# Performance work log

Hardware: AMD Instinct MI355X
Metric: run time of the kernel (lower is better)

Reference implementation:

```python
import jax, jax.numpy as jnp
import numpy as np

D_MODEL = 1024
NUM_HEADS = 16
HEAD_DIM = D_MODEL // NUM_HEADS  # 64
SEQ = 2048
BATCH = 4
LN_EPS = 1e-5


def setup_inputs() -> dict:
    key = jax.random.key(0)
    k_in, k_qkv, k_o, k_g = jax.random.split(key, 4)
    inputs = jax.random.normal(k_in, (BATCH, SEQ, D_MODEL), dtype=jnp.float32)
    mask = jnp.zeros((BATCH, 1, SEQ, SEQ), dtype=jnp.float32)  # additive mask
    # Realistic rotary embeddings (RoPE), duplicated-halves layout
    inv_freq = 1.0 / (10000.0 ** (jnp.arange(0, HEAD_DIM, 2, dtype=jnp.float32) / HEAD_DIM))
    pos = jnp.arange(SEQ, dtype=jnp.float32)
    freqs = pos[:, None] * inv_freq[None, :]            # [S, Dh/2]
    emb = jnp.concatenate([freqs, freqs], axis=-1)       # [S, Dh]
    cos = jnp.cos(emb)
    sin = jnp.sin(emb)
    # Parameters
    sd = 1.0 / np.sqrt(D_MODEL)
    w_qkv = jax.random.normal(k_qkv, (D_MODEL, 3 * D_MODEL), dtype=jnp.float32) * sd
    w_o = jax.random.normal(k_o, (D_MODEL, D_MODEL), dtype=jnp.float32) * sd
    ln_gamma = jnp.ones((D_MODEL,), dtype=jnp.float32)
    return {"inputs": inputs, "mask": mask, "cos": cos, "sin": sin,
            "ln_gamma": ln_gamma, "w_qkv": w_qkv, "w_o": w_o}


def _rotate_half(x):
    x1, x2 = jnp.split(x, 2, axis=-1)
    return jnp.concatenate([-x2, x1], axis=-1)


def reference(inputs, mask, cos, sin, ln_gamma, w_qkv, w_o):
    B, S, D = inputs.shape
    # Pre-attention LayerNorm (layer_id != 0), center=False -> no beta
    mu = jnp.mean(inputs, axis=-1, keepdims=True)
    var = jnp.mean(jnp.square(inputs - mu), axis=-1, keepdims=True)
    x = (inputs - mu) / jnp.sqrt(var + LN_EPS) * ln_gamma
    # Fused QKV projection, split into heads: [B, H, S, Dh]
    qkv = (x @ w_qkv).reshape(B, S, 3, NUM_HEADS, HEAD_DIM)
    qkv = jnp.transpose(qkv, (2, 0, 3, 1, 4))
    q, k, v = qkv[0], qkv[1], qkv[2]
    # RoPE
    c = cos.reshape(1, 1, S, HEAD_DIM)
    s = sin.reshape(1, 1, S, HEAD_DIM)
    q = q * c + _rotate_half(q) * s
    k = k * c + _rotate_half(k) * s
    # Scaled dot-product attention with additive mask
    scale = 1.0 / jnp.sqrt(jnp.asarray(HEAD_DIM, dtype=q.dtype))
    logits = jnp.einsum("bhqd,bhkd->bhqk", q, k) * scale + mask
    attn = jax.nn.softmax(logits, axis=-1)
    out = jnp.einsum("bhqk,bhkd->bhqd", attn, v)
    out = jnp.transpose(out, (0, 2, 1, 3)).reshape(B, S, D)
    return out @ w_o
```

## Files before the change

kernel.cpp:

```cpp
#include <hip/hip_runtime.h>
#include <stdint.h>

#define DEV __device__ __forceinline__

typedef __bf16 bf16x8 __attribute__((ext_vector_type(8)));
typedef float f32x4 __attribute__((ext_vector_type(4)));
typedef float f32x16 __attribute__((ext_vector_type(16)));

DEV unsigned short f2bf(float f) {
  union { float f; uint32_t u; } c; c.f = f;
  uint32_t u = c.u;
  u += 0x7FFFu + ((u >> 16) & 1u);
  return (unsigned short)(u >> 16);
}
DEV float bf2f(unsigned short h) {
  union { uint32_t u; float f; } c; c.u = ((uint32_t)h) << 16;
  return c.f;
}
DEV float u2f(uint32_t u) {
  union { uint32_t u; float f; } c; c.u = u;
  return c.f;
}
DEV bf16x8 ld8(const unsigned short* p) {
  uint4 u = *reinterpret_cast<const uint4*>(p);
  return __builtin_bit_cast(bf16x8, u);
}
DEV uint32_t cvtpk(float lo, float hi) {
  uint32_t r;
  asm("v_cvt_pk_bf16_f32 %0, %1, %2" : "=v"(r) : "v"(lo), "v"(hi));
  return r;
}
DEV void permswap(uint32_t& a, uint32_t& b) {
  asm("v_permlane32_swap_b32 %0, %1" : "+v"(a), "+v"(b));
}
DEV float exp2b(float x) { return __builtin_amdgcn_exp2f(x); }
DEV void gload16(const void* g, void* l) {
  __builtin_amdgcn_global_load_lds((const __attribute__((address_space(1))) void*)g,
                                   (__attribute__((address_space(3))) void*)l, 16, 0, 0);
}

template<int K, int N>
__global__ __launch_bounds__(256)
void transpose_cast_kernel(const float* __restrict__ in, unsigned short* __restrict__ out) {
  __shared__ float tile[64][65];
  const int bk = blockIdx.x % (K / 64);
  const int bn = blockIdx.x / (K / 64);
  const int k0 = bk * 64, n0 = bn * 64;
  const int t = threadIdx.x;
#pragma unroll
  for (int i = 0; i < 16; ++i) {
    int idx = t + i * 256;
    int kl = idx >> 6, nl = idx & 63;
    tile[kl][nl] = in[(size_t)(k0 + kl) * N + n0 + nl];
  }
  __syncthreads();
#pragma unroll
  for (int i = 0; i < 16; ++i) {
    int idx = t + i * 256;
    int nl = idx >> 6, kl = idx & 63;
    out[(size_t)(n0 + nl) * K + k0 + kl] = f2bf(tile[kl][nl]);
  }
}

__global__ __launch_bounds__(256)
void ln_kernel(const float* __restrict__ x, const float* __restrict__ gamma,
               unsigned short* __restrict__ y) {
  const int row = blockIdx.x;
  const int t = threadIdx.x;
  const float4 v = reinterpret_cast<const float4*>(x + (size_t)row * 1024)[t];
  float s  = v.x + v.y + v.z + v.w;
  float s2 = v.x * v.x + v.y * v.y + v.z * v.z + v.w * v.w;
#pragma unroll
  for (int off = 1; off < 64; off <<= 1) {
    s  += __shfl_xor(s, off);
    s2 += __shfl_xor(s2, off);
  }
  __shared__ float red[8];
  const int w = t >> 6, lane = t & 63;
  if (lane == 0) { red[w] = s; red[4 + w] = s2; }
  __syncthreads();
  s  = red[0] + red[1] + red[2] + red[3];
  s2 = red[4] + red[5] + red[6] + red[7];
  const float mu = s * (1.0f / 1024.0f);
  const float var = s2 * (1.0f / 1024.0f) - mu * mu;
  const float rstd = rsqrtf(var + 1e-5f);
  const float4 g = reinterpret_cast<const float4*>(gamma)[t];
  ushort4 o;
  o.x = f2bf((v.x - mu) * rstd * g.x);
  o.y = f2bf((v.y - mu) * rstd * g.y);
  o.z = f2bf((v.z - mu) * rstd * g.z);
  o.w = f2bf((v.w - mu) * rstd * g.w);
  reinterpret_cast<ushort4*>(y + (size_t)row * 1024)[t] = o;
}

template<int N_DIM, bool OUT_F32>
__global__ __launch_bounds__(256)
void gemm_bt_kernel(const unsigned short* __restrict__ A,
                    const unsigned short* __restrict__ Bt,
                    void* __restrict__ Cout) {
  constexpr int K = 1024;
  __shared__ unsigned short a_lds[128 * 32];
  __shared__ unsigned short b_lds[128 * 32];
  const int t = threadIdx.x;
  const int w = t >> 6, l = t & 63;
  const int lrow = l & 15, lch = l >> 4;
  const int nbn = N_DIM / 128;
  const int m0 = (blockIdx.x / nbn) * 128;
  const int n0 = (blockIdx.x % nbn) * 128;
  const int wm = (w >> 1) * 64, wn = (w & 1) * 64;

  const int srow = t >> 2;
  const int schk = t & 3;
  const int scol = ((schk ^ (srow & 3)) << 3);
  const unsigned short* aS0 = A  + (size_t)(m0 + srow) * K + scol;
  const unsigned short* aS1 = A  + (size_t)(m0 + 64 + srow) * K + scol;
  const unsigned short* bS0 = Bt + (size_t)(n0 + srow) * K + scol;
  const unsigned short* bS1 = Bt + (size_t)(n0 + 64 + srow) * K + scol;
  unsigned short* aD0 = a_lds + (w * 16) * 32;
  unsigned short* aD1 = a_lds + (64 + w * 16) * 32;
  unsigned short* bD0 = b_lds + (w * 16) * 32;
  unsigned short* bD1 = b_lds + (64 + w * 16) * 32;

  f32x4 acc[4][4] = {};

  for (int k0 = 0; k0 < K; k0 += 32) {
    gload16(aS0 + k0, aD0);
    gload16(aS1 + k0, aD1);
    gload16(bS0 + k0, bD0);
    gload16(bS1 + k0, bD1);
    __syncthreads();
    bf16x8 af[4], bfr[4];
#pragma unroll
    for (int m = 0; m < 4; ++m) {
      int row = wm + m * 16 + lrow;
      af[m] = ld8(a_lds + row * 32 + ((lch ^ (lrow & 3)) << 3));
    }
#pragma unroll
    for (int n = 0; n < 4; ++n) {
      int row = wn + n * 16 + lrow;
      bfr[n] = ld8(b_lds + row * 32 + ((lch ^ (lrow & 3)) << 3));
    }
#pragma unroll
    for (int m = 0; m < 4; ++m)
#pragma unroll
      for (int n = 0; n < 4; ++n)
        acc[m][n] = __builtin_amdgcn_mfma_f32_16x16x32_bf16(af[m], bfr[n], acc[m][n], 0, 0, 0);
    __syncthreads();
  }

#pragma unroll
  for (int m = 0; m < 4; ++m) {
    const int grow0 = m0 + wm + m * 16 + lch * 4;
#pragma unroll
    for (int n = 0; n < 4; ++n) {
      const int gcol = n0 + wn + n * 16 + lrow;
#pragma unroll
      for (int r = 0; r < 4; ++r) {
        if constexpr (OUT_F32)
          ((float*)Cout)[(size_t)(grow0 + r) * N_DIM + gcol] = acc[m][n][r];
        else
          ((unsigned short*)Cout)[(size_t)(grow0 + r) * N_DIM + gcol] = f2bf(acc[m][n][r]);
      }
    }
  }
}

__global__ __launch_bounds__(256)
void rope_split_kernel(const unsigned short* __restrict__ qkv,
                       const float* __restrict__ cosb,
                       const float* __restrict__ sinb,
                       unsigned short* __restrict__ Qo,
                       unsigned short* __restrict__ Kf,
                       unsigned short* __restrict__ Vf) {
  const int bid = blockIdx.x;
  const int sb = bid & 31, h = (bid >> 5) & 15, b = bid >> 9;
  const int s0 = sb * 64;
  const int t = threadIdx.x;
  __shared__ unsigned short qt[64][72], kt[64][72], vt[64][72];

  const int sl = t >> 2, c0 = (t & 3) * 16;
  {
    const size_t base = (size_t)(b * 2048 + s0 + sl) * 3072 + h * 64 + c0;
    uint4 q1 = *(const uint4*)(qkv + base);
    uint4 q2 = *(const uint4*)(qkv + base + 8);
    uint4 k1 = *(const uint4*)(qkv + base + 1024);
    uint4 k2 = *(const uint4*)(qkv + base + 1032);
    uint4 v1 = *(const uint4*)(qkv + base + 2048);
    uint4 v2 = *(const uint4*)(qkv + base + 2056);
    *(uint4*)&qt[sl][c0] = q1; *(uint4*)&qt[sl][c0 + 8] = q2;
    *(uint4*)&kt[sl][c0] = k1; *(uint4*)&kt[sl][c0 + 8] = k2;
    *(uint4*)&vt[sl][c0] = v1; *(uint4*)&vt[sl][c0 + 8] = v2;
  }
  __syncthreads();
  const size_t fbase = (size_t)(b * 16 + h) * 131072;
  {
    const int sg = s0 + sl;
    alignas(16) unsigned short qo16[16], ko16[16];
#pragma unroll
    for (int j = 0; j < 16; ++j) {
      const int d = c0 + j;
      const float cv = cosb[sg * 64 + d], sv = sinb[sg * 64 + d];
      const float qv = bf2f(qt[sl][d]), qp = bf2f(qt[sl][d ^ 32]);
      const float kv = bf2f(kt[sl][d]), kp = bf2f(kt[sl][d ^ 32]);
      const float rq = qv * cv + ((d < 32) ? -qp : qp) * sv;
      const float rk = kv * cv + ((d < 32) ? -kp : kp) * sv;
      qo16[j] = f2bf(rq * 0.180336880f);
      ko16[j] = f2bf(rk);
    }
    const size_t ob = ((size_t)(b * 16 + h) * 2048 + sg) * 64 + c0;
    *(uint4*)(Qo + ob) = *(uint4*)qo16; *(uint4*)(Qo + ob + 8) = *(uint4*)(qo16 + 8);
    unsigned short* kd = Kf + fbase + ((size_t)((sb * 2 + (sl >> 5)) * 4 + (t & 3))) * 512;
    *(uint4*)(kd + (sl & 31) * 8)        = *(uint4*)ko16;
    *(uint4*)(kd + (32 + (sl & 31)) * 8) = *(uint4*)(ko16 + 8);
  }
  {
    const int dh = t >> 2, sc0 = (t & 3) * 16;
    alignas(16) unsigned short vo16[16];
#pragma unroll
    for (int j = 0; j < 16; ++j) vo16[j] = vt[sc0 + j][dh];
    unsigned short* vd = Vf + fbase + ((size_t)((sb * 2 + (dh >> 5)) * 4 + (t & 3))) * 512;
    *(uint4*)(vd + (dh & 31) * 8)        = *(uint4*)vo16;
    *(uint4*)(vd + (32 + (dh & 31)) * 8) = *(uint4*)(vo16 + 8);
  }
}

__global__ __launch_bounds__(256)
void mask_prep_kernel(const float* __restrict__ mask, unsigned short* __restrict__ mrs,
                      unsigned char* __restrict__ flg) {
  const int bid = blockIdx.x;
  const int kvt = bid & 31, qc = (bid >> 5) & 31, b = bid >> 10;
  const int t = threadIdx.x;
  __shared__ float tile[64][72];
  __shared__ int nzf;
  if (t == 0) nzf = 0;
  uint32_t orbits = 0;
  {
    const int r = t >> 2, c0 = (t & 3) * 16;
    const float* src = mask + (size_t)b * (2048ull * 2048) + (size_t)(qc * 64 + r) * 2048 + kvt * 64 + c0;
#pragma unroll
    for (int i = 0; i < 4; ++i) {
      const float4 v = *(const float4*)(src + i * 4);
      *(float4*)&tile[r][c0 + i * 4] = v;
      orbits |= __float_as_uint(v.x) | __float_as_uint(v.y) |
                __float_as_uint(v.z) | __float_as_uint(v.w);
    }
  }
  __syncthreads();
  if (orbits != 0u) nzf = 1;
  __syncthreads();
  if (nzf) {
    const int cid = t >> 5;
    const int n = cid >> 2, jj = (cid >> 1) & 1, hi = cid & 1;
    const int qq0 = (t & 31) * 2;
    const int cb = n * 32 + jj * 16 + hi * 4;
    unsigned short* dst = mrs + (((size_t)(b * 32 + kvt) * 8 + cid) * 2048 + qc * 64) * 8;
#pragma unroll
    for (int qo = 0; qo < 2; ++qo) {
      const int q = qq0 + qo;
      alignas(16) unsigned short o8[8];
#pragma unroll
      for (int v = 0; v < 8; ++v) {
        const int col = cb + (v >> 2) * 8 + (v & 3);
        o8[v] = f2bf(tile[q][col] * 1.44269504f);
      }
      *(uint4*)(dst + (size_t)q * 8) = *(uint4*)o8;
    }
  }
  if (t == 0) flg[(size_t)(b * 32 + kvt) * 32 + qc] = (unsigned char)nzf;
}

__global__ __launch_bounds__(256)
void attn_kernel(const unsigned short* __restrict__ Q,
                 const unsigned short* __restrict__ Kf,
                 const unsigned short* __restrict__ Vf,
                 const unsigned short* __restrict__ mrs,
                 const unsigned char* __restrict__ flg,
                 unsigned short* __restrict__ O) {
  const int t = threadIdx.x, w = t >> 6, l = t & 63;
  const int lq = l & 31, hi = l >> 5;
  const int bid = blockIdx.x;
  const int x = bid & 7, y = bid >> 3;
  const int bh = x * 8 + (y & 7), qb = y >> 3;
  const int b = bh >> 4, h = bh & 15;
  const int q0 = qb * 128 + w * 32;

  const unsigned short* Qb  = Q  + (size_t)bh * (2048 * 64);
  const unsigned short* Kfb = Kf + (size_t)bh * 131072;
  const unsigned short* Vfb = Vf + (size_t)bh * 131072;
  const unsigned short* ml = mrs + (size_t)b * 4194304 + (size_t)hi * 16384 + (size_t)(q0 + lq) * 8;
  const unsigned char* fb = flg + (size_t)(b * 32) * 32 + qb * 2;

  bf16x8 qf[4];
  {
    const unsigned short* qp = Qb + (size_t)(q0 + lq) * 64 + hi * 8;
#pragma unroll
    for (int c = 0; c < 4; ++c) qf[c] = ld8(qp + c * 16);
  }
  bf16x8 ones;
  {
    const uint4 ou = { 0x3F803F80u, 0x3F803F80u, 0x3F803F80u, 0x3F803F80u };
    ones = __builtin_bit_cast(bf16x8, ou);
  }

  f32x16 ot0 = {}, ot1 = {};
  f32x16 st_sum = {};

  uint4 mA[4], mB[4];

  auto do_tile = [&](int kvt, uint4 (&mcur)[4], uint4 (&mnext)[4],
                     bool hm, bool hmn) {
    const unsigned short* kp = Kfb + (size_t)kvt * 4096 + l * 8;
    const unsigned short* vp = Vfb + (size_t)kvt * 4096 + l * 8;
    uint4 kr[8], vr[8];
#pragma unroll
    for (int i = 0; i < 8; ++i) kr[i] = *(const uint4*)(kp + i * 512);
#pragma unroll
    for (int i = 0; i < 8; ++i) vr[i] = *(const uint4*)(vp + i * 512);

    const bool more = (kvt + 1) < 32;
    if (more && hmn) {
      const unsigned short* mp = ml + (size_t)(kvt + 1) * 131072;
#pragma unroll
      for (int c2 = 0; c2 < 4; ++c2) mnext[c2] = *(const uint4*)(mp + c2 * 32768);
    }

    f32x16 st0 = {}, st1 = {};
    if (hm) {
#pragma unroll
      for (int jj = 0; jj < 2; ++jj) {
        const uint4 u0 = mcur[jj];
        const uint4 u1 = mcur[2 + jj];
#pragma unroll
        for (int wv = 0; wv < 4; ++wv) {
          const uint32_t w0 = ((const uint32_t*)&u0)[wv];
          const uint32_t w1 = ((const uint32_t*)&u1)[wv];
          st0[jj * 8 + wv * 2]     = u2f(w0 << 16);
          st0[jj * 8 + wv * 2 + 1] = u2f(w0 & 0xffff0000u);
          st1[jj * 8 + wv * 2]     = u2f(w1 << 16);
          st1[jj * 8 + wv * 2 + 1] = u2f(w1 & 0xffff0000u);
        }
      }
    }

    __builtin_amdgcn_s_setprio(1);
#pragma unroll
    for (int c = 0; c < 4; ++c) {
      st0 = __builtin_amdgcn_mfma_f32_32x32x16_bf16(__builtin_bit_cast(bf16x8, kr[c]),     qf[c], st0, 0, 0, 0);
      st1 = __builtin_amdgcn_mfma_f32_32x32x16_bf16(__builtin_bit_cast(bf16x8, kr[4 + c]), qf[c], st1, 0, 0, 0);
    }
    __builtin_amdgcn_s_setprio(0);

#pragma unroll
    for (int r = 0; r < 16; ++r) {
      st0[r] = exp2b(st0[r]);
      st1[r] = exp2b(st1[r]);
    }

    bf16x8 pa[4];
#pragma unroll
    for (int c = 0; c < 4; ++c) {
      const int e8 = (c & 1) * 8;
      uint32_t A01, B01, A23, B23;
      if (c < 2) {
        A01 = cvtpk(st0[e8 + 0], st0[e8 + 1]);
        B01 = cvtpk(st0[e8 + 4], st0[e8 + 5]);
        A23 = cvtpk(st0[e8 + 2], st0[e8 + 3]);
        B23 = cvtpk(st0[e8 + 6], st0[e8 + 7]);
      } else {
        A01 = cvtpk(st1[e8 + 0], st1[e8 + 1]);
        B01 = cvtpk(st1[e8 + 4], st1[e8 + 5]);
        A23 = cvtpk(st1[e8 + 2], st1[e8 + 3]);
        B23 = cvtpk(st1[e8 + 6], st1[e8 + 7]);
      }
      permswap(A01, B01);
      permswap(A23, B23);
      const uint4 pw = { A01, A23, B01, B23 };
      pa[c] = __builtin_bit_cast(bf16x8, pw);
    }

    __builtin_amdgcn_s_setprio(1);
#pragma unroll
    for (int c = 0; c < 4; ++c) {
      ot0 = __builtin_amdgcn_mfma_f32_32x32x16_bf16(__builtin_bit_cast(bf16x8, vr[c]),     pa[c], ot0, 0, 0, 0);
      ot1 = __builtin_amdgcn_mfma_f32_32x32x16_bf16(__builtin_bit_cast(bf16x8, vr[4 + c]), pa[c], ot1, 0, 0, 0);
      st_sum = __builtin_amdgcn_mfma_f32_32x32x16_bf16(ones, pa[c], st_sum, 0, 0, 0);
    }
    __builtin_amdgcn_s_setprio(0);
  };

  unsigned int bm = 0;
  for (int kvt = 0; kvt < 32; ++kvt) bm |= fb[kvt * 32] | fb[kvt * 32 + 1];

  if (bm == 0) {
    for (int kvt = 0; kvt < 32; kvt += 2) {
      do_tile(kvt, mA, mB, false, false);
      do_tile(kvt + 1, mB, mA, false, false);
    }
  } else {
    bool hmA = (fb[0] | fb[1]) != 0;
    if (hmA) {
#pragma unroll
      for (int c2 = 0; c2 < 4; ++c2) mA[c2] = *(const uint4*)(ml + c2 * 32768);
    }
    bool hmB = false;
    for (int kvt = 0; kvt < 32; kvt += 2) {
      hmB = (kvt + 1 < 32) && ((fb[(kvt + 1) * 32] | fb[(kvt + 1) * 32 + 1]) != 0);
      do_tile(kvt, mA, mB, hmA, hmB);
      const bool hmA2 = (kvt + 2 < 32) && ((fb[(kvt + 2) * 32] | fb[(kvt + 2) * 32 + 1]) != 0);
      do_tile(kvt + 1, mB, mA, hmB, hmA2);
      hmA = hmA2;
    }
  }

  const float inv = 1.0f / st_sum[0];
  unsigned short* ob = O + ((size_t)(b * 2048 + q0 + lq) * 16 + h) * 64 + hi * 4;
#pragma unroll
  for (int td = 0; td < 2; ++td) {
#pragma unroll
    for (int rr = 0; rr < 4; ++rr) {
      ushort4 ov;
      if (td == 0) {
        ov.x = f2bf(ot0[rr * 4 + 0] * inv);
        ov.y = f2bf(ot0[rr * 4 + 1] * inv);
        ov.z = f2bf(ot0[rr * 4 + 2] * inv);
        ov.w = f2bf(ot0[rr * 4 + 3] * inv);
      } else {
        ov.x = f2bf(ot1[rr * 4 + 0] * inv);
        ov.y = f2bf(ot1[rr * 4 + 1] * inv);
        ov.z = f2bf(ot1[rr * 4 + 2] * inv);
        ov.w = f2bf(ot1[rr * 4 + 3] * inv);
      }
      *(ushort4*)(ob + td * 32 + rr * 8) = ov;
    }
  }
}

extern "C" void kernel_launch(void* const* d_in, const int* in_sizes, int n_in,
                              void* d_out, int out_size, void* d_ws, size_t ws_size,
                              hipStream_t stream) {
  (void)in_sizes; (void)n_in; (void)out_size; (void)ws_size;
  const float* x     = (const float*)d_in[0];
  const float* mask  = (const float*)d_in[1];
  const float* cosb  = (const float*)d_in[2];
  const float* sinb  = (const float*)d_in[3];
  const float* gamma = (const float*)d_in[4];
  const float* w_qkv = (const float*)d_in[5];
  const float* w_o   = (const float*)d_in[6];

  char* ws = (char*)d_ws;
  unsigned short* x_bf   = (unsigned short*)(ws);
  unsigned short* wqkvT  = (unsigned short*)(ws + 16777216);
  unsigned short* woT    = (unsigned short*)(ws + 23068672);
  unsigned short* qkv_bf = (unsigned short*)(ws + 25165824);
  unsigned short* q_r    = (unsigned short*)(ws + 75497472);
  unsigned short* k_f    = (unsigned short*)(ws + 92274688);
  unsigned short* v_f    = (unsigned short*)(ws + 109051904);
  unsigned short* attn   = (unsigned short*)(ws + 125829120);
  unsigned short* mask_rs = qkv_bf;
  unsigned char*  flags   = (unsigned char*)(ws + 25165824 + 33554432);

  transpose_cast_kernel<1024, 3072><<<dim3(16 * 48), dim3(256), 0, stream>>>(w_qkv, wqkvT);
  transpose_cast_kernel<1024, 1024><<<dim3(16 * 16), dim3(256), 0, stream>>>(w_o, woT);
  ln_kernel<<<dim3(8192), dim3(256), 0, stream>>>(x, gamma, x_bf);
  gemm_bt_kernel<3072, false><<<dim3(64 * 24), dim3(256), 0, stream>>>(x_bf, wqkvT, (void*)qkv_bf);
  rope_split_kernel<<<dim3(4 * 16 * 32), dim3(256), 0, stream>>>(qkv_bf, cosb, sinb, q_r, k_f, v_f);
  mask_prep_kernel<<<dim3(4096), dim3(256), 0, stream>>>(mask, mask_rs, flags);
  attn_kernel<<<dim3(1024), dim3(256), 0, stream>>>(q_r, k_f, v_f, mask_rs, flags, attn);
  gemm_bt_kernel<1024, true><<<dim3(64 * 8), dim3(256), 0, stream>>>(attn, woT, d_out);
}
```

Baseline: 260.8 us.

## Prefetch next K tile across iterations and reorder block-to-head mapping

The attention kernel now double-buffers K register tiles, loading tile kvt+1 while computing tile kvt, so the QK MFMAs no longer wait on a fresh global load. Mask loads change from prefetched to loaded on demand, which is cheap when the mask is all zeros, and the flag check becomes a single bitmask with one unified loop. The block index mapping also changes so that consecutive blocks cover the q-blocks of the same head, which may improve L2 reuse of K and V. The cost is higher register pressure from holding two K buffers, which could lower occupancy.

```diff
diff --git a/kernel.cpp b/kernel.cpp
--- a/kernel.cpp
+++ b/kernel.cpp
@@ -280,13 +280,14 @@
   const int lq = l & 31, hi = l >> 5;
   const int bid = blockIdx.x;
   const int x = bid & 7, y = bid >> 3;
-  const int bh = x * 8 + (y & 7), qb = y >> 3;
+  const int bh = x * 8 + (y >> 4);
+  const int qb = y & 15;
   const int b = bh >> 4, h = bh & 15;
   const int q0 = qb * 128 + w * 32;
 
   const unsigned short* Qb  = Q  + (size_t)bh * (2048 * 64);
-  const unsigned short* Kfb = Kf + (size_t)bh * 131072;
-  const unsigned short* Vfb = Vf + (size_t)bh * 131072;
+  const unsigned short* Kfb = Kf + (size_t)bh * 131072 + l * 8;
+  const unsigned short* Vfb = Vf + (size_t)bh * 131072 + l * 8;
   const unsigned short* ml = mrs + (size_t)b * 4194304 + (size_t)hi * 16384 + (size_t)(q0 + lq) * 8;
   const unsigned char* fb = flg + (size_t)(b * 32) * 32 + qb * 2;
 
@@ -305,31 +306,35 @@
   f32x16 ot0 = {}, ot1 = {};
   f32x16 st_sum = {};
 
-  uint4 mA[4], mB[4];
-
-  auto do_tile = [&](int kvt, uint4 (&mcur)[4], uint4 (&mnext)[4],
-                     bool hm, bool hmn) {
-    const unsigned short* kp = Kfb + (size_t)kvt * 4096 + l * 8;
-    const unsigned short* vp = Vfb + (size_t)kvt * 4096 + l * 8;
-    uint4 kr[8], vr[8];
-#pragma unroll
-    for (int i = 0; i < 8; ++i) kr[i] = *(const uint4*)(kp + i * 512);
+  unsigned int bmap = 0;
+  for (int kvt = 0; kvt < 32; ++kvt)
+    if (fb[kvt * 32] | fb[kvt * 32 + 1]) bmap |= (1u << kvt);
+
+  uint4 krA[8], krB[8];
+#pragma unroll
+  for (int i = 0; i < 8; ++i) krA[i] = *(const uint4*)(Kfb + i * 512);
+
+  auto do_tile = [&](int kvt, uint4 (&ckr)[8], uint4 (&nkr)[8], bool hm) {
+    if (kvt + 1 < 32) {
+      const unsigned short* kp = Kfb + (size_t)(kvt + 1) * 4096;
+#pragma unroll
+      for (int i = 0; i < 8; ++i) nkr[i] = *(const uint4*)(kp + i * 512);
+    }
+    const unsigned short* vp = Vfb + (size_t)kvt * 4096;
+    uint4 vr[8];
 #pragma unroll
     for (int i = 0; i < 8; ++i) vr[i] = *(const uint4*)(vp + i * 512);
-
-    const bool more = (kvt + 1) < 32;
-    if (more && hmn) {
-      const unsigned short* mp = ml + (size_t)(kvt + 1) * 131072;
-#pragma unroll
-      for (int c2 = 0; c2 < 4; ++c2) mnext[c2] = *(const uint4*)(mp + c2 * 32768);
-    }
 
     f32x16 st0 = {}, st1 = {};
     if (hm) {
+      const unsigned short* mp = ml + (size_t)kvt * 131072;
+      uint4 mc[4];
+#pragma unroll
+      for (int c2 = 0; c2 < 4; ++c2) mc[c2] = *(const uint4*)(mp + c2 * 32768);
 #pragma unroll
       for (int jj = 0; jj < 2; ++jj) {
-        const uint4 u0 = mcur[jj];
-        const uint4 u1 = mcur[2 + jj];
+        const uint4 u0 = mc[jj];
+        const uint4 u1 = mc[2 + jj];
 #pragma unroll
         for (int wv = 0; wv < 4; ++wv) {
           const uint32_t w0 = ((const uint32_t*)&u0)[wv];
@@ -345,8 +350,8 @@
     __builtin_amdgcn_s_setprio(1);
 #pragma unroll
     for (int c = 0; c < 4; ++c) {
-      st0 = __builtin_amdgcn_mfma_f32_32x32x16_bf16(__builtin_bit_cast(bf16x8, kr[c]),     qf[c], st0, 0, 0, 0);
-      st1 = __builtin_amdgcn_mfma_f32_32x32x16_bf16(__builtin_bit_cast(bf16x8, kr[4 + c]), qf[c], st1, 0, 0, 0);
+      st0 = __builtin_amdgcn_mfma_f32_32x32x16_bf16(__builtin_bit_cast(bf16x8, ckr[c]),     qf[c], st0, 0, 0, 0);
+      st1 = __builtin_amdgcn_mfma_f32_32x32x16_bf16(__builtin_bit_cast(bf16x8, ckr[4 + c]), qf[c], st1, 0, 0, 0);
     }
     __builtin_amdgcn_s_setprio(0);
 
@@ -388,28 +393,9 @@
     __builtin_amdgcn_s_setprio(0);
   };
 
-  unsigned int bm = 0;
-  for (int kvt = 0; kvt < 32; ++kvt) bm |= fb[kvt * 32] | fb[kvt * 32 + 1];
-
-  if (bm == 0) {
-    for (int kvt = 0; kvt < 32; kvt += 2) {
-      do_tile(kvt, mA, mB, false, false);
-      do_tile(kvt + 1, mB, mA, false, false);
-    }
-  } else {
-    bool hmA = (fb[0] | fb[1]) != 0;
-    if (hmA) {
-#pragma unroll
-      for (int c2 = 0; c2 < 4; ++c2) mA[c2] = *(const uint4*)(ml + c2 * 32768);
-    }
-    bool hmB = false;
-    for (int kvt = 0; kvt < 32; kvt += 2) {
-      hmB = (kvt + 1 < 32) && ((fb[(kvt + 1) * 32] | fb[(kvt + 1) * 32 + 1]) != 0);
-      do_tile(kvt, mA, mB, hmA, hmB);
-      const bool hmA2 = (kvt + 2 < 32) && ((fb[(kvt + 2) * 32] | fb[(kvt + 2) * 32 + 1]) != 0);
-      do_tile(kvt + 1, mB, mA, hmB, hmA2);
-      hmA = hmA2;
-    }
+  for (int kvt = 0; kvt < 32; kvt += 2) {
+    do_tile(kvt,     krA, krB, (bmap >> kvt) & 1u);
+    do_tile(kvt + 1, krB, krA, (bmap >> (kvt + 1)) & 1u);
   }
 
   const float inv = 1.0f / st_sum[0];
```

Result: no change. 257.6 us (-1.2%).
